# Kernel tuning notes

Measured on AMD Instinct MI355X. Metric: run time of the kernel, lower is better.

## Reference

```python
import jax, jax.numpy as jnp
import numpy as np

B, S_DEC, S_ENC, D, H = 2, 2048, 2048, 1024, 16
HD = D // H  # 64


def setup_inputs() -> dict:
    key = jax.random.key(0)
    ks = jax.random.split(key, 12)
    s = 0.02
    return {
        "dec_hidden_state": jax.random.normal(ks[0], (B, S_DEC, D), jnp.float32),
        "enc_hidden_state": jax.random.normal(ks[1], (B, S_ENC, D), jnp.float32),
        "mask": jnp.ones((B, S_ENC, S_DEC), jnp.int32),
        "Wq": jax.random.normal(ks[2], (H, D, HD), jnp.float32) * s,
        "bq": jax.random.normal(ks[3], (H, HD), jnp.float32) * s,
        "Wk": jax.random.normal(ks[4], (H, D, HD), jnp.float32) * s,
        "bk": jax.random.normal(ks[5], (H, HD), jnp.float32) * s,
        "Wv": jax.random.normal(ks[6], (H, D, HD), jnp.float32) * s,
        "bv": jax.random.normal(ks[7], (H, HD), jnp.float32) * s,
        "Wo": jax.random.normal(ks[8], (D, D), jnp.float32) * s,
        "bo": jax.random.normal(ks[9], (D,), jnp.float32) * s,
    }


def reference(dec_hidden_state, enc_hidden_state, mask, Wq, bq, Wk, bk, Wv, bv, Wo, bo):
    # NOTE: original module swaps args: query <- enc_hidden_state, key/value <- dec_hidden_state.
    # q: [B,H,S_enc,HD], k/v: [B,H,S_dec,HD]
    q = jnp.einsum("bqd,hdk->bhqk", enc_hidden_state, Wq) + bq[None, :, None, :]
    k = jnp.einsum("bsd,hdk->bhsk", dec_hidden_state, Wk) + bk[None, :, None, :]
    v = jnp.einsum("bsd,hdk->bhsk", dec_hidden_state, Wv) + bv[None, :, None, :]
    scores = jnp.einsum("bhqk,bhsk->bhqs", q, k) / jnp.sqrt(jnp.asarray(HD, q.dtype))
    scores = jnp.where(mask[:, None, :, :] == 0, jnp.asarray(-jnp.inf, scores.dtype), scores)
    weights = jax.nn.softmax(scores, axis=-1)
    attn = jnp.einsum("bhqs,bhsk->bhqk", weights, v)  # [B,H,S_enc,HD]
    # concat heads along last dim (same order as torch.cat over head list)
    attn = jnp.transpose(attn, (0, 2, 1, 3)).reshape(B, S_ENC, D)
    return attn @ Wo + bo
```

## Files before the change

kernel.cpp:

```cpp
#include <hip/hip_runtime.h>
#include <math.h>
#include <stdint.h>


typedef unsigned short ushort_t;
typedef __attribute__((ext_vector_type(8))) short short8;
typedef __attribute__((ext_vector_type(4))) short short4v;
typedef __attribute__((ext_vector_type(4))) float floatx4;

__device__ __forceinline__ ushort_t f2bf(float x){
  unsigned u = __float_as_uint(x);
  u += 0x7fffu + ((u >> 16) & 1u);
  return (ushort_t)(u >> 16);
}
__device__ __forceinline__ unsigned pk2bf(float a, float b){
#if __has_builtin(__builtin_amdgcn_cvt_pk_bf16_f32)
  typedef __attribute__((ext_vector_type(2))) __bf16 bf2_t;
  bf2_t r = __builtin_amdgcn_cvt_pk_bf16_f32(a, b);
  return *(unsigned*)&r;
#else
  return (unsigned)f2bf(a) | ((unsigned)f2bf(b) << 16);
#endif
}
__device__ __forceinline__ floatx4 mfma16(short8 a, short8 b, floatx4 c){
  return __builtin_amdgcn_mfma_f32_16x16x32_bf16(a, b, c, 0, 0, 0);
}
#if __has_builtin(__builtin_amdgcn_mfma_f32_16x16x16bf16_1k)
__device__ __forceinline__ floatx4 mfma_pv(short4v a, short4v b, floatx4 c){
  return __builtin_amdgcn_mfma_f32_16x16x16bf16_1k(a, b, c, 0, 0, 0);
}
#else
__device__ __forceinline__ floatx4 mfma_pv(short4v a, short4v b, floatx4 c){
  short8 a8 = {a[0], a[1], a[2], a[3], 0, 0, 0, 0};
  short8 b8 = {b[0], b[1], b[2], b[3], 0, 0, 0, 0};
  return mfma16(a8, b8, c);
}
#endif
__device__ __forceinline__ void async_copy16(const void* g, void* l){
  __builtin_amdgcn_global_load_lds((const __attribute__((address_space(1))) void*)g,
                                   (__attribute__((address_space(3))) void*)l,
                                   16, 0, 0);
}

__global__ __launch_bounds__(256)
void prep_kernel(const float* __restrict__ enc, const float* __restrict__ dec,
                 const float* __restrict__ Wq, const float* __restrict__ Wk,
                 const float* __restrict__ Wv, const float* __restrict__ Wo,
                 const int* __restrict__ mask,
                 ushort_t* __restrict__ encb, ushort_t* __restrict__ decb,
                 ushort_t* __restrict__ WqT, ushort_t* __restrict__ WkT,
                 ushort_t* __restrict__ WvT, ushort_t* __restrict__ WoT,
                 unsigned long long* __restrict__ mb)
{
  __shared__ float t[64][65];
  const int bx = blockIdx.x, tid = threadIdx.x;
  if (bx < 8192){
    const float* src = (bx < 4096) ? enc : dec;
    ushort_t*    dst = (bx < 4096) ? encb : decb;
    int i = ((bx & 4095) * 256 + tid) * 4;
    const float4 v = *(const float4*)(src + i);
    unsigned long long p = (unsigned long long)f2bf(v.x)
                         | ((unsigned long long)f2bf(v.y) << 16)
                         | ((unsigned long long)f2bf(v.z) << 32)
                         | ((unsigned long long)f2bf(v.w) << 48);
    *(unsigned long long*)(dst + i) = p;
  } else if (bx < 8960){
    const int id = bx - 8192;
    const int zz = id >> 4, yy = id & 15;
    const int which = zz >> 4, head = zz & 15;
    const float* src = (which == 0) ? Wq : (which == 1) ? Wk : Wv;
    ushort_t*    dst = (which == 0) ? WqT : (which == 1) ? WkT : WvT;
    const long sb = (long)head * 65536;
    const int r0 = yy * 64;
    #pragma unroll
    for (int i = 0; i < 16; i++){
      int idx = i*256 + tid;
      int r = idx >> 6, c = idx & 63;
      t[r][c] = src[sb + (long)(r0 + r)*64 + c];
    }
    __syncthreads();
    #pragma unroll
    for (int i = 0; i < 16; i++){
      int idx = i*256 + tid;
      int cr = idx >> 6, rc = idx & 63;
      dst[sb + (long)cr*1024 + r0 + rc] = f2bf(t[rc][cr]);
    }
  } else if (bx < 9216){
    const int id = bx - 8960;
    const int r0 = (id >> 4) * 64, c0 = (id & 15) * 64;
    #pragma unroll
    for (int i = 0; i < 16; i++){
      int idx = i*256 + tid;
      int r = idx >> 6, c = idx & 63;
      t[r][c] = Wo[(long)(r0 + r)*1024 + c0 + c];
    }
    __syncthreads();
    #pragma unroll
    for (int i = 0; i < 16; i++){
      int idx = i*256 + tid;
      int cr = idx >> 6, rc = idx & 63;
      WoT[(long)(c0 + cr)*1024 + r0 + rc] = f2bf(t[rc][cr]);
    }
  } else {
    long gid = (long)(bx - 9216) * 256 + tid;
    unsigned long long bal = __ballot(mask[gid] != 0);
    if ((tid & 63) == 0) mb[gid >> 6] = bal;
  }
}

__global__ __launch_bounds__(256, 3)
void gemm_qkv_kernel(const ushort_t* __restrict__ encb, const ushort_t* __restrict__ decb,
                     const ushort_t* __restrict__ WqT, const ushort_t* __restrict__ WkT,
                     const ushort_t* __restrict__ WvT,
                     const float* __restrict__ bq, const float* __restrict__ bk,
                     const float* __restrict__ bv,
                     ushort_t* __restrict__ Qb, ushort_t* __restrict__ Kbf,
                     ushort_t* __restrict__ Vtb)
{
  __shared__ ushort_t At[2*4096];
  __shared__ ushort_t Bt[2*4096];
  const int tid = threadIdx.x;
  const int wave = tid >> 6, lane = tid & 63;
  const int quad = lane >> 4, l16 = lane & 15;
  const int z = blockIdx.z;
  const ushort_t *A, *BT; const float* bias; ushort_t* outp;
  int m0, n0; long outAdj = 0;
  if (z == 0){ A = encb; BT = WqT; bias = bq; outp = Qb;  m0 = blockIdx.y*128; n0 = blockIdx.x*128; }
  else if (z == 1){ A = decb; BT = WkT; bias = bk; outp = Kbf; m0 = blockIdx.y*128; n0 = blockIdx.x*128; }
  else {
    int id = blockIdx.y*8 + blockIdx.x;
    int vb = id >> 7, rem = id & 127;
    m0 = ((rem >> 4) & 7) * 128; n0 = (rem & 15) * 128;
    A = WvT; BT = decb + (long)vb*2097152; bias = bv; outp = Vtb; outAdj = (long)vb*2097152;
  }
  const int K = 1024;

  const int c0 = tid, c1 = 256 + tid;
  const ushort_t* gA0 = A  + (long)(m0 + (c0 >> 2))*K + (c0 & 3)*8;
  const ushort_t* gA1 = A  + (long)(m0 + (c1 >> 2))*K + (c1 & 3)*8;
  const ushort_t* gB0 = BT + (long)(n0 + (c0 >> 2))*K + (c0 & 3)*8;
  const ushort_t* gB1 = BT + (long)(n0 + (c1 >> 2))*K + (c1 & 3)*8;

  floatx4 acc[4][4];
  #pragma unroll
  for (int mt = 0; mt < 4; mt++)
    #pragma unroll
    for (int nt = 0; nt < 4; nt++)
      acc[mt][nt] = (floatx4){0.f, 0.f, 0.f, 0.f};

  async_copy16(gA0, &At[wave*512]);
  async_copy16(gA1, &At[(4+wave)*512]);
  async_copy16(gB0, &Bt[wave*512]);
  async_copy16(gB1, &Bt[(4+wave)*512]);
  gA0 += 32; gA1 += 32; gB0 += 32; gB1 += 32;

  const int moff = (wave & 1) * 64, noff = (wave >> 1) * 64;
  int cur = 0;
  for (int k0 = 0; k0 < K; k0 += 32){
    __syncthreads();
    if (k0 + 32 < K){
      const int nx = cur ^ 1;
      async_copy16(gA0, &At[nx*4096 + wave*512]);
      async_copy16(gA1, &At[nx*4096 + (4+wave)*512]);
      async_copy16(gB0, &Bt[nx*4096 + wave*512]);
      async_copy16(gB1, &Bt[nx*4096 + (4+wave)*512]);
      gA0 += 32; gA1 += 32; gB0 += 32; gB1 += 32;
    }
    short8 af[4], bfr[4];
    #pragma unroll
    for (int t = 0; t < 4; t++){
      af[t]  = *(const short8*)&At[cur*4096 + (moff + t*16 + l16)*32 + quad*8];
      bfr[t] = *(const short8*)&Bt[cur*4096 + (noff + t*16 + l16)*32 + quad*8];
    }
    #pragma unroll
    for (int mt = 0; mt < 4; mt++)
      #pragma unroll
      for (int nt = 0; nt < 4; nt++)
        acc[mt][nt] = mfma16(bfr[nt], af[mt], acc[mt][nt]);
    cur ^= 1;
  }

  #pragma unroll
  for (int mt = 0; mt < 4; mt++){
    #pragma unroll
    for (int nt = 0; nt < 4; nt++){
      floatx4 v = acc[mt][nt];
      if (z < 2){
        const int s   = m0 + moff + mt*16 + l16;
        const int ch0 = n0 + noff + nt*16 + quad*4;
        const float4 b4 = *(const float4*)&bias[ch0];
        uint2 pk;
        pk.x = pk2bf(v[0] + b4.x, v[1] + b4.y);
        pk.y = pk2bf(v[2] + b4.z, v[3] + b4.w);
        *(unsigned long long*)&outp[(long)s*1024 + ch0] = *(unsigned long long*)&pk;
      } else {
        const int ch = m0 + moff + mt*16 + l16;
        const int s0 = n0 + noff + nt*16 + quad*4;
        const float bb = bias[ch];
        uint2 pk;
        pk.x = pk2bf(v[0] + bb, v[1] + bb);
        pk.y = pk2bf(v[2] + bb, v[3] + bb);
        *(unsigned long long*)&outp[outAdj + (long)ch*2048 + s0] = *(unsigned long long*)&pk;
      }
    }
  }
}

__global__ __launch_bounds__(256, 2)
void gemm_o_kernel(const ushort_t* __restrict__ A, const ushort_t* __restrict__ BT,
                   const float* __restrict__ bias, float* __restrict__ outf)
{
  __shared__ ushort_t At[2*4096];
  __shared__ ushort_t Bt[2*2048];
  const int tid = threadIdx.x;
  const int wave = tid >> 6, lane = tid & 63;
  const int quad = lane >> 4, l16 = lane & 15;
  const int m0 = blockIdx.y * 128, n0 = blockIdx.x * 64;
  const int K = 1024;

  const int c0 = tid, c1 = 256 + tid;
  const ushort_t* gA0 = A  + (long)(m0 + (c0 >> 2))*K + (c0 & 3)*8;
  const ushort_t* gA1 = A  + (long)(m0 + (c1 >> 2))*K + (c1 & 3)*8;
  const ushort_t* gB0 = BT + (long)(n0 + (c0 >> 2))*K + (c0 & 3)*8;

  floatx4 acc[4][2];
  #pragma unroll
  for (int mt = 0; mt < 4; mt++)
    #pragma unroll
    for (int nt = 0; nt < 2; nt++)
      acc[mt][nt] = (floatx4){0.f, 0.f, 0.f, 0.f};

  async_copy16(gA0, &At[wave*512]);
  async_copy16(gA1, &At[(4+wave)*512]);
  async_copy16(gB0, &Bt[wave*512]);
  gA0 += 32; gA1 += 32; gB0 += 32;

  const int moff = (wave & 1) * 64, noff = (wave >> 1) * 32;
  int cur = 0;
  for (int k0 = 0; k0 < K; k0 += 32){
    __syncthreads();
    if (k0 + 32 < K){
      const int nx = cur ^ 1;
      async_copy16(gA0, &At[nx*4096 + wave*512]);
      async_copy16(gA1, &At[nx*4096 + (4+wave)*512]);
      async_copy16(gB0, &Bt[nx*2048 + wave*512]);
      gA0 += 32; gA1 += 32; gB0 += 32;
    }
    short8 af[4], bfr[2];
    #pragma unroll
    for (int t = 0; t < 4; t++)
      af[t]  = *(const short8*)&At[cur*4096 + (moff + t*16 + l16)*32 + quad*8];
    #pragma unroll
    for (int t = 0; t < 2; t++)
      bfr[t] = *(const short8*)&Bt[cur*2048 + (noff + t*16 + l16)*32 + quad*8];
    #pragma unroll
    for (int mt = 0; mt < 4; mt++)
      #pragma unroll
      for (int nt = 0; nt < 2; nt++)
        acc[mt][nt] = mfma16(bfr[nt], af[mt], acc[mt][nt]);
    cur ^= 1;
  }

  #pragma unroll
  for (int mt = 0; mt < 4; mt++){
    #pragma unroll
    for (int nt = 0; nt < 2; nt++){
      const int s   = m0 + moff + mt*16 + l16;
      const int ch0 = n0 + noff + nt*16 + quad*4;
      const float4 b4 = *(const float4*)&bias[ch0];
      float4 o;
      o.x = acc[mt][nt][0] + b4.x;
      o.y = acc[mt][nt][1] + b4.y;
      o.z = acc[mt][nt][2] + b4.z;
      o.w = acc[mt][nt][3] + b4.w;
      *(float4*)&outf[(long)s*1024 + ch0] = o;
    }
  }
}

__global__ __launch_bounds__(256, 4)
void flash_attn_kernel(const ushort_t* __restrict__ Qp, const ushort_t* __restrict__ Kp,
                       const ushort_t* __restrict__ Vt, const unsigned* __restrict__ mb,
                       ushort_t* __restrict__ aout)
{
  __shared__ ushort_t Kbuf[2*4608];
  __shared__ ushort_t Vbuf[2*4608];
  const int tid = threadIdx.x, wave = tid >> 6, lane = tid & 63;
  const int quad = lane >> 4, l16 = lane & 15;
  const int bh = blockIdx.x, qt = blockIdx.y;
  const int b = bh >> 4, h = bh & 15;
  const float C = 0.18033688011112042f;

  const ushort_t* VB = Vt + (long)bh*131072;
  const int q0 = qt*64 + wave*16;

  const long qrow = ((long)b*2048 + q0 + l16)*1024 + h*64;
  short8 qf0 = *(const short8*)&Qp[qrow +      quad*8];
  short8 qf1 = *(const short8*)&Qp[qrow + 32 + quad*8];

  floatx4 accO[4];
  #pragma unroll
  for (int ht = 0; ht < 4; ht++) accO[ht] = (floatx4){0.f,0.f,0.f,0.f};
  float lsum = 0.f;

  const int c0 = tid, c1 = 256 + tid;
  const ushort_t* gK0 = Kp + ((long)b*2048 + (c0 >> 3))*1024 + h*64 + (c0 & 7)*8;
  const ushort_t* gK1 = Kp + ((long)b*2048 + (c1 >> 3))*1024 + h*64 + (c1 & 7)*8;
  const ushort_t* gV0 = VB + (long)(c0 >> 3)*2048 + (c0 & 7)*8;
  const ushort_t* gV1 = VB + (long)(c1 >> 3)*2048 + (c1 & 7)*8;
  const int lo0 = (c0 >> 3)*72 + (c0 & 7)*8;
  const int lo1 = (c1 >> 3)*72 + (c1 & 7)*8;

  const uint2* mb2 = (const uint2*)mb;
  const long mbase = (long)b*2048 + q0;

  short8 gk0 = *(const short8*)gK0;  gK0 += 65536;
  short8 gk1 = *(const short8*)gK1;  gK1 += 65536;
  short8 gv0 = *(const short8*)gV0;  gV0 += 64;
  short8 gv1 = *(const short8*)gV1;  gV1 += 64;

  int cur = 0;
  for (int st = 0; st < 32; st++){
    *(short8*)&Kbuf[cur*4608 + lo0] = gk0;
    *(short8*)&Kbuf[cur*4608 + lo1] = gk1;
    *(short8*)&Vbuf[cur*4608 + lo0] = gv0;
    *(short8*)&Vbuf[cur*4608 + lo1] = gv1;
    __syncthreads();
    if (st < 31){
      gk0 = *(const short8*)gK0;  gK0 += 65536;
      gk1 = *(const short8*)gK1;  gK1 += 65536;
      gv0 = *(const short8*)gV0;  gV0 += 64;
      gv1 = *(const short8*)gV1;  gV1 += 64;
    }
    const ushort_t* Kt = &Kbuf[cur*4608];
    const ushort_t* Vp = &Vbuf[cur*4608];

    uint2 mw = mb2[(mbase + l16)*32 + st];
    const bool uni = __all((mw.x & mw.y) == 0xFFFFFFFFu);

    #pragma unroll
    for (int mtile = 0; mtile < 4; mtile++){
      short8 kf0 = *(const short8*)&Kt[(mtile*16 + l16)*72 +      quad*8];
      short8 kf1 = *(const short8*)&Kt[(mtile*16 + l16)*72 + 32 + quad*8];
      floatx4 zz = (floatx4){0.f,0.f,0.f,0.f};
      zz = mfma16(kf0, qf0, zz);
      zz = mfma16(kf1, qf1, zz);
      float p0 = __builtin_amdgcn_exp2f(zz[0]*C);
      float p1 = __builtin_amdgcn_exp2f(zz[1]*C);
      float p2 = __builtin_amdgcn_exp2f(zz[2]*C);
      float p3 = __builtin_amdgcn_exp2f(zz[3]*C);
      if (__builtin_expect(!uni, 0)){
        const unsigned w = (mtile & 2) ? mw.y : mw.x;
        const int sh = (mtile & 1)*16 + quad*4;
        p0 = ((w >> (sh+0)) & 1u) ? p0 : 0.f;
        p1 = ((w >> (sh+1)) & 1u) ? p1 : 0.f;
        p2 = ((w >> (sh+2)) & 1u) ? p2 : 0.f;
        p3 = ((w >> (sh+3)) & 1u) ? p3 : 0.f;
      }
      lsum += (p0 + p1) + (p2 + p3);
      uint2 pk; pk.x = pk2bf(p0, p1); pk.y = pk2bf(p2, p3);
      const short4v pb = *(const short4v*)&pk;
      #pragma unroll
      for (int ht = 0; ht < 4; ht++){
        short4v vf = *(const short4v*)&Vp[(ht*16 + l16)*72 + mtile*16 + quad*4];
        accO[ht] = mfma_pv(vf, pb, accO[ht]);
      }
    }
    cur ^= 1;
  }

  lsum += __shfl_xor(lsum, 16);
  lsum += __shfl_xor(lsum, 32);
  const float inv = 1.0f / lsum;

  const long rowo = ((long)b*2048 + q0 + l16)*1024 + h*64;
  #pragma unroll
  for (int ht = 0; ht < 4; ht++){
    uint2 pk;
    pk.x = pk2bf(accO[ht][0]*inv, accO[ht][1]*inv);
    pk.y = pk2bf(accO[ht][2]*inv, accO[ht][3]*inv);
    *(unsigned long long*)&aout[rowo + ht*16 + quad*4] = *(unsigned long long*)&pk;
  }
}

extern "C" void kernel_launch(void* const* d_in, const int* in_sizes, int n_in,
                              void* d_out, int out_size, void* d_ws, size_t ws_size,
                              hipStream_t stream) {
  const float* dec  = (const float*)d_in[0];
  const float* enc  = (const float*)d_in[1];
  const int*   mask = (const int*)d_in[2];
  const float* Wq   = (const float*)d_in[3];
  const float* bq   = (const float*)d_in[4];
  const float* Wk   = (const float*)d_in[5];
  const float* bk   = (const float*)d_in[6];
  const float* Wv   = (const float*)d_in[7];
  const float* bv   = (const float*)d_in[8];
  const float* Wo   = (const float*)d_in[9];
  const float* bo   = (const float*)d_in[10];
  float* out = (float*)d_out;

  ushort_t* ws   = (ushort_t*)d_ws;
  ushort_t* encb = ws;
  ushort_t* decb = encb + 4194304;
  ushort_t* Qb   = decb + 4194304;
  ushort_t* Kbf  = Qb   + 4194304;
  ushort_t* Vtb  = Kbf  + 4194304;
  ushort_t* WqT  = Vtb  + 4194304;
  ushort_t* WkT  = WqT  + 1048576;
  ushort_t* WvT  = WkT  + 1048576;
  ushort_t* WoT  = WvT  + 1048576;
  unsigned* Mb   = (unsigned*)(WoT + 1048576);

  prep_kernel<<<41984, 256, 0, stream>>>(enc, dec, Wq, Wk, Wv, Wo, mask,
                                         encb, decb, WqT, WkT, WvT, WoT,
                                         (unsigned long long*)Mb);
  gemm_qkv_kernel<<<dim3(8,32,3), 256, 0, stream>>>(encb, decb, WqT, WkT, WvT,
                                                    bq, bk, bv, Qb, Kbf, Vtb);
  flash_attn_kernel<<<dim3(32,32,1), 256, 0, stream>>>(Qb, Kbf, Vtb, Mb, encb);
  gemm_o_kernel<<<dim3(16,32,1), 256, 0, stream>>>(encb, WoT, bo, out);
}
```

Before: 258.3 us.

## Double flash-attn query rows per wave, fold softmax scale into Q, register-staged GEMM loads

Flash attention now processes two 16-row query tiles per wave, reusing each loaded K and V fragment across both tiles and halving the grid. The softmax scale constant moves into the Q projection epilogue, removing a multiply per score. The GEMM kernels replace direct global-to-LDS async copies with register-staged loads and stores into LDS, and swap grid axes to change block ordering. Register pressure rises in the attention kernel, and occupancy is relaxed to match.

```diff
diff --git a/kernel.cpp b/kernel.cpp
--- a/kernel.cpp
+++ b/kernel.cpp
@@ -36,11 +36,6 @@
   return mfma16(a8, b8, c);
 }
 #endif
-__device__ __forceinline__ void async_copy16(const void* g, void* l){
-  __builtin_amdgcn_global_load_lds((const __attribute__((address_space(1))) void*)g,
-                                   (__attribute__((address_space(3))) void*)l,
-                                   16, 0, 0);
-}
 
 __global__ __launch_bounds__(256)
 void prep_kernel(const float* __restrict__ enc, const float* __restrict__ dec,
@@ -125,10 +120,12 @@
   const int z = blockIdx.z;
   const ushort_t *A, *BT; const float* bias; ushort_t* outp;
   int m0, n0; long outAdj = 0;
-  if (z == 0){ A = encb; BT = WqT; bias = bq; outp = Qb;  m0 = blockIdx.y*128; n0 = blockIdx.x*128; }
-  else if (z == 1){ A = decb; BT = WkT; bias = bk; outp = Kbf; m0 = blockIdx.y*128; n0 = blockIdx.x*128; }
+  float qs = 1.0f;
+  if (z == 0){ A = encb; BT = WqT; bias = bq; outp = Qb;  m0 = blockIdx.x*128; n0 = blockIdx.y*128;
+               qs = 0.18033688011112042f; }
+  else if (z == 1){ A = decb; BT = WkT; bias = bk; outp = Kbf; m0 = blockIdx.x*128; n0 = blockIdx.y*128; }
   else {
-    int id = blockIdx.y*8 + blockIdx.x;
+    int id = blockIdx.x*8 + blockIdx.y;
     int vb = id >> 7, rem = id & 127;
     m0 = ((rem >> 4) & 7) * 128; n0 = (rem & 15) * 128;
     A = WvT; BT = decb + (long)vb*2097152; bias = bv; outp = Vtb; outAdj = (long)vb*2097152;
@@ -148,23 +145,24 @@
     for (int nt = 0; nt < 4; nt++)
       acc[mt][nt] = (floatx4){0.f, 0.f, 0.f, 0.f};
 
-  async_copy16(gA0, &At[wave*512]);
-  async_copy16(gA1, &At[(4+wave)*512]);
-  async_copy16(gB0, &Bt[wave*512]);
-  async_copy16(gB1, &Bt[(4+wave)*512]);
-  gA0 += 32; gA1 += 32; gB0 += 32; gB1 += 32;
+  short8 rA0 = *(const short8*)gA0;  gA0 += 32;
+  short8 rA1 = *(const short8*)gA1;  gA1 += 32;
+  short8 rB0 = *(const short8*)gB0;  gB0 += 32;
+  short8 rB1 = *(const short8*)gB1;  gB1 += 32;
 
   const int moff = (wave & 1) * 64, noff = (wave >> 1) * 64;
   int cur = 0;
   for (int k0 = 0; k0 < K; k0 += 32){
+    *(short8*)&At[cur*4096 +        tid*8] = rA0;
+    *(short8*)&At[cur*4096 + 2048 + tid*8] = rA1;
+    *(short8*)&Bt[cur*4096 +        tid*8] = rB0;
+    *(short8*)&Bt[cur*4096 + 2048 + tid*8] = rB1;
     __syncthreads();
     if (k0 + 32 < K){
-      const int nx = cur ^ 1;
-      async_copy16(gA0, &At[nx*4096 + wave*512]);
-      async_copy16(gA1, &At[nx*4096 + (4+wave)*512]);
-      async_copy16(gB0, &Bt[nx*4096 + wave*512]);
-      async_copy16(gB1, &Bt[nx*4096 + (4+wave)*512]);
-      gA0 += 32; gA1 += 32; gB0 += 32; gB1 += 32;
+      rA0 = *(const short8*)gA0;  gA0 += 32;
+      rA1 = *(const short8*)gA1;  gA1 += 32;
+      rB0 = *(const short8*)gB0;  gB0 += 32;
+      rB1 = *(const short8*)gB1;  gB1 += 32;
     }
     short8 af[4], bfr[4];
     #pragma unroll
@@ -190,8 +188,8 @@
         const int ch0 = n0 + noff + nt*16 + quad*4;
         const float4 b4 = *(const float4*)&bias[ch0];
         uint2 pk;
-        pk.x = pk2bf(v[0] + b4.x, v[1] + b4.y);
-        pk.y = pk2bf(v[2] + b4.z, v[3] + b4.w);
+        pk.x = pk2bf((v[0] + b4.x)*qs, (v[1] + b4.y)*qs);
+        pk.y = pk2bf((v[2] + b4.z)*qs, (v[3] + b4.w)*qs);
         *(unsigned long long*)&outp[(long)s*1024 + ch0] = *(unsigned long long*)&pk;
       } else {
         const int ch = m0 + moff + mt*16 + l16;
@@ -215,7 +213,7 @@
   const int tid = threadIdx.x;
   const int wave = tid >> 6, lane = tid & 63;
   const int quad = lane >> 4, l16 = lane & 15;
-  const int m0 = blockIdx.y * 128, n0 = blockIdx.x * 64;
+  const int m0 = blockIdx.x * 128, n0 = blockIdx.y * 64;
   const int K = 1024;
 
   const int c0 = tid, c1 = 256 + tid;
@@ -230,21 +228,21 @@
     for (int nt = 0; nt < 2; nt++)
       acc[mt][nt] = (floatx4){0.f, 0.f, 0.f, 0.f};
 
-  async_copy16(gA0, &At[wave*512]);
-  async_copy16(gA1, &At[(4+wave)*512]);
-  async_copy16(gB0, &Bt[wave*512]);
-  gA0 += 32; gA1 += 32; gB0 += 32;
+  short8 rA0 = *(const short8*)gA0;  gA0 += 32;
+  short8 rA1 = *(const short8*)gA1;  gA1 += 32;
+  short8 rB0 = *(const short8*)gB0;  gB0 += 32;
 
   const int moff = (wave & 1) * 64, noff = (wave >> 1) * 32;
   int cur = 0;
   for (int k0 = 0; k0 < K; k0 += 32){
+    *(short8*)&At[cur*4096 +        tid*8] = rA0;
+    *(short8*)&At[cur*4096 + 2048 + tid*8] = rA1;
+    *(short8*)&Bt[cur*2048 +        tid*8] = rB0;
     __syncthreads();
     if (k0 + 32 < K){
-      const int nx = cur ^ 1;
-      async_copy16(gA0, &At[nx*4096 + wave*512]);
-      async_copy16(gA1, &At[nx*4096 + (4+wave)*512]);
-      async_copy16(gB0, &Bt[nx*2048 + wave*512]);
-      gA0 += 32; gA1 += 32; gB0 += 32;
+      rA0 = *(const short8*)gA0;  gA0 += 32;
+      rA1 = *(const short8*)gA1;  gA1 += 32;
+      rB0 = *(const short8*)gB0;  gB0 += 32;
     }
     short8 af[4], bfr[2];
     #pragma unroll
@@ -278,7 +276,7 @@
   }
 }
 
-__global__ __launch_bounds__(256, 4)
+__global__ __launch_bounds__(256, 2)
 void flash_attn_kernel(const ushort_t* __restrict__ Qp, const ushort_t* __restrict__ Kp,
                        const ushort_t* __restrict__ Vt, const unsigned* __restrict__ mb,
                        ushort_t* __restrict__ aout)
@@ -289,19 +287,24 @@
   const int quad = lane >> 4, l16 = lane & 15;
   const int bh = blockIdx.x, qt = blockIdx.y;
   const int b = bh >> 4, h = bh & 15;
-  const float C = 0.18033688011112042f;
 
   const ushort_t* VB = Vt + (long)bh*131072;
-  const int q0 = qt*64 + wave*16;
-
-  const long qrow = ((long)b*2048 + q0 + l16)*1024 + h*64;
-  short8 qf0 = *(const short8*)&Qp[qrow +      quad*8];
-  short8 qf1 = *(const short8*)&Qp[qrow + 32 + quad*8];
-
-  floatx4 accO[4];
-  #pragma unroll
-  for (int ht = 0; ht < 4; ht++) accO[ht] = (floatx4){0.f,0.f,0.f,0.f};
-  float lsum = 0.f;
+  const int q0 = qt*128 + wave*32;
+
+  short8 qf[2][2];
+  #pragma unroll
+  for (int mtq = 0; mtq < 2; mtq++){
+    const long qrow = ((long)b*2048 + q0 + mtq*16 + l16)*1024 + h*64;
+    qf[mtq][0] = *(const short8*)&Qp[qrow +      quad*8];
+    qf[mtq][1] = *(const short8*)&Qp[qrow + 32 + quad*8];
+  }
+
+  floatx4 accO[2][4];
+  #pragma unroll
+  for (int mtq = 0; mtq < 2; mtq++)
+    #pragma unroll
+    for (int ht = 0; ht < 4; ht++) accO[mtq][ht] = (floatx4){0.f,0.f,0.f,0.f};
+  float lsum[2] = {0.f, 0.f};
 
   const int c0 = tid, c1 = 256 + tid;
   const ushort_t* gK0 = Kp + ((long)b*2048 + (c0 >> 3))*1024 + h*64 + (c0 & 7)*8;
@@ -335,51 +338,65 @@
     const ushort_t* Kt = &Kbuf[cur*4608];
     const ushort_t* Vp = &Vbuf[cur*4608];
 
-    uint2 mw = mb2[(mbase + l16)*32 + st];
-    const bool uni = __all((mw.x & mw.y) == 0xFFFFFFFFu);
+    uint2 mw[2];
+    #pragma unroll
+    for (int mtq = 0; mtq < 2; mtq++)
+      mw[mtq] = mb2[(mbase + mtq*16 + l16)*32 + st];
+    const bool uni = __all((mw[0].x & mw[0].y & mw[1].x & mw[1].y) == 0xFFFFFFFFu);
 
     #pragma unroll
     for (int mtile = 0; mtile < 4; mtile++){
       short8 kf0 = *(const short8*)&Kt[(mtile*16 + l16)*72 +      quad*8];
       short8 kf1 = *(const short8*)&Kt[(mtile*16 + l16)*72 + 32 + quad*8];
-      floatx4 zz = (floatx4){0.f,0.f,0.f,0.f};
-      zz = mfma16(kf0, qf0, zz);
-      zz = mfma16(kf1, qf1, zz);
-      float p0 = __builtin_amdgcn_exp2f(zz[0]*C);
-      float p1 = __builtin_amdgcn_exp2f(zz[1]*C);
-      float p2 = __builtin_amdgcn_exp2f(zz[2]*C);
-      float p3 = __builtin_amdgcn_exp2f(zz[3]*C);
-      if (__builtin_expect(!uni, 0)){
-        const unsigned w = (mtile & 2) ? mw.y : mw.x;
-        const int sh = (mtile & 1)*16 + quad*4;
-        p0 = ((w >> (sh+0)) & 1u) ? p0 : 0.f;
-        p1 = ((w >> (sh+1)) & 1u) ? p1 : 0.f;
-        p2 = ((w >> (sh+2)) & 1u) ? p2 : 0.f;
-        p3 = ((w >> (sh+3)) & 1u) ? p3 : 0.f;
+      short4v vf[4];
+      #pragma unroll
+      for (int ht = 0; ht < 4; ht++)
+        vf[ht] = *(const short4v*)&Vp[(ht*16 + l16)*72 + mtile*16 + quad*4];
+      #pragma unroll
+      for (int mtq = 0; mtq < 2; mtq++){
+        floatx4 zz = (floatx4){0.f,0.f,0.f,0.f};
+        zz = mfma16(kf0, qf[mtq][0], zz);
+        zz = mfma16(kf1, qf[mtq][1], zz);
+        float p0 = __builtin_amdgcn_exp2f(zz[0]);
+        float p1 = __builtin_amdgcn_exp2f(zz[1]);
+        float p2 = __builtin_amdgcn_exp2f(zz[2]);
+        float p3 = __builtin_amdgcn_exp2f(zz[3]);
+        if (__builtin_expect(!uni, 0)){
+          const unsigned w = (mtile & 2) ? mw[mtq].y : mw[mtq].x;
+          const int sh = (mtile & 1)*16 + quad*4;
+          p0 = ((w >> (sh+0)) & 1u) ? p0 : 0.f;
+          p1 = ((w >> (sh+1)) & 1u) ? p1 : 0.f;
+          p2 = ((w >> (sh+2)) & 1u) ? p2 : 0.f;
+          p3 = ((w >> (sh+3)) & 1u) ? p3 : 0.f;
+        }
+        lsum[mtq] += (p0 + p1) + (p2 + p3);
+        uint2 pk; pk.x = pk2bf(p0, p1); pk.y = pk2bf(p2, p3);
+        const short4v pb = *(const short4v*)&pk;
+        #pragma unroll
+        for (int ht = 0; ht < 4; ht++)
+          accO[mtq][ht] = mfma_pv(vf[ht], pb, accO[mtq][ht]);
       }
-      lsum += (p0 + p1) + (p2 + p3);
-      uint2 pk; pk.x = pk2bf(p0, p1); pk.y = pk2bf(p2, p3);
-      const short4v pb = *(const short4v*)&pk;
-      #pragma unroll
-      for (int ht = 0; ht < 4; ht++){
-        short4v vf = *(const short4v*)&Vp[(ht*16 + l16)*72 + mtile*16 + quad*4];
-        accO[ht] = mfma_pv(vf, pb, accO[ht]);
-      }
     }
     cur ^= 1;
   }
 
-  lsum += __shfl_xor(lsum, 16);
-  lsum += __shfl_xor(lsum, 32);
-  const float inv = 1.0f / lsum;
-
-  const long rowo = ((long)b*2048 + q0 + l16)*1024 + h*64;
-  #pragma unroll
-  for (int ht = 0; ht < 4; ht++){
-    uint2 pk;
-    pk.x = pk2bf(accO[ht][0]*inv, accO[ht][1]*inv);
-    pk.y = pk2bf(accO[ht][2]*inv, accO[ht][3]*inv);
-    *(unsigned long long*)&aout[rowo + ht*16 + quad*4] = *(unsigned long long*)&pk;
+  #pragma unroll
+  for (int mtq = 0; mtq < 2; mtq++){
+    lsum[mtq] += __shfl_xor(lsum[mtq], 16);
+    lsum[mtq] += __shfl_xor(lsum[mtq], 32);
+  }
+
+  #pragma unroll
+  for (int mtq = 0; mtq < 2; mtq++){
+    const float inv = 1.0f / lsum[mtq];
+    const long rowo = ((long)b*2048 + q0 + mtq*16 + l16)*1024 + h*64;
+    #pragma unroll
+    for (int ht = 0; ht < 4; ht++){
+      uint2 pk;
+      pk.x = pk2bf(accO[mtq][ht][0]*inv, accO[mtq][ht][1]*inv);
+      pk.y = pk2bf(accO[mtq][ht][2]*inv, accO[mtq][ht][3]*inv);
+      *(unsigned long long*)&aout[rowo + ht*16 + quad*4] = *(unsigned long long*)&pk;
+    }
   }
 }
 
@@ -414,8 +431,8 @@
   prep_kernel<<<41984, 256, 0, stream>>>(enc, dec, Wq, Wk, Wv, Wo, mask,
                                          encb, decb, WqT, WkT, WvT, WoT,
                                          (unsigned long long*)Mb);
-  gemm_qkv_kernel<<<dim3(8,32,3), 256, 0, stream>>>(encb, decb, WqT, WkT, WvT,
+  gemm_qkv_kernel<<<dim3(32,8,3), 256, 0, stream>>>(encb, decb, WqT, WkT, WvT,
                                                     bq, bk, bv, Qb, Kbf, Vtb);
-  flash_attn_kernel<<<dim3(32,32,1), 256, 0, stream>>>(Qb, Kbf, Vtb, Mb, encb);
-  gemm_o_kernel<<<dim3(16,32,1), 256, 0, stream>>>(encb, WoT, bo, out);
-}
+  flash_attn_kernel<<<dim3(32,16,1), 256, 0, stream>>>(Qb, Kbf, Vtb, Mb, encb);
+  gemm_o_kernel<<<dim3(32,16,1), 256, 0, stream>>>(encb, WoT, bo, out);
+}
```

After: 258.0 us. No clear change (-0.1%).
